# Optimization experiments

Measured on AMD Instinct MI355X. Metric: run time of the kernel, lower is better.

The kernel has to match this reference:

```python
import jax, jax.numpy as jnp
import numpy as np

N = 50000
D_IN = 256
OUT = 16
HEADS = 32
GAT_C = OUT  # out_channels + beta_on(=0)


def _gat_conv(x, src, dst, W, att_src, att_dst, bias):
    """PyG GATConv, concat=False (mean over heads), with self-loops already appended."""
    n = x.shape[0]
    xp = (x @ W).reshape(n, HEADS, GAT_C)            # [N,H,C]
    a_s = jnp.einsum('nhc,hc->nh', xp, att_src)       # [N,H]
    a_d = jnp.einsum('nhc,hc->nh', xp, att_dst)       # [N,H]
    e = jax.nn.leaky_relu(a_s[src] + a_d[dst], 0.2)   # [E,H]
    # segment softmax over incoming edges of each dst node
    m = jax.ops.segment_max(e, dst, num_segments=n)
    e = jnp.exp(e - m[dst])
    s = jax.ops.segment_sum(e, dst, num_segments=n)
    alpha = e / (s[dst] + 1e-16)                      # [E,H]
    out = jax.ops.segment_sum(alpha[:, :, None] * xp[src], dst, num_segments=n)  # [N,H,C]
    return out.mean(axis=1) + bias                    # [N,C]


def setup_inputs() -> dict:
    key = jax.random.key(0)
    ks = jax.random.split(key, 16)
    E = 800000
    x = jax.random.normal(ks[0], (N, D_IN), dtype=jnp.float32)
    edge_index = jax.random.randint(ks[1], (2, E), 0, N, dtype=jnp.int64)
    sc = 1.0 / np.sqrt(D_IN)
    W1 = jax.random.normal(ks[2], (D_IN, HEADS * GAT_C), dtype=jnp.float32) * sc
    att_src1 = jax.random.normal(ks[3], (HEADS, GAT_C), dtype=jnp.float32) * 0.1
    att_dst1 = jax.random.normal(ks[4], (HEADS, GAT_C), dtype=jnp.float32) * 0.1
    b1 = jnp.zeros((GAT_C,), dtype=jnp.float32)
    W2 = jax.random.normal(ks[5], (D_IN, HEADS * GAT_C), dtype=jnp.float32) * sc
    att_src2 = jax.random.normal(ks[6], (HEADS, GAT_C), dtype=jnp.float32) * 0.1
    att_dst2 = jax.random.normal(ks[7], (HEADS, GAT_C), dtype=jnp.float32) * 0.1
    b2 = jnp.zeros((GAT_C,), dtype=jnp.float32)
    lin1_w = jax.random.normal(ks[8], (D_IN, 4 * OUT), dtype=jnp.float32) * sc
    lin1_b = jnp.zeros((4 * OUT,), dtype=jnp.float32)
    lin2_w = jax.random.normal(ks[9], (4 * OUT, OUT), dtype=jnp.float32) * (1.0 / np.sqrt(4 * OUT))
    lin2_b = jnp.zeros((OUT,), dtype=jnp.float32)
    return {"x": x, "edge_index": edge_index,
            "W1": W1, "att_src1": att_src1, "att_dst1": att_dst1, "b1": b1,
            "W2": W2, "att_src2": att_src2, "att_dst2": att_dst2, "b2": b2,
            "lin1_w": lin1_w, "lin1_b": lin1_b, "lin2_w": lin2_w, "lin2_b": lin2_b}


def reference(x, edge_index, W1, att_src1, att_dst1, b1, W2, att_src2, att_dst2, b2,
              lin1_w, lin1_b, lin2_w, lin2_b):
    n = x.shape[0]
    loops = jnp.arange(n, dtype=edge_index.dtype)
    # conv1: flow source_to_target on edge_index -> aggregate src=row0 into dst=row1
    src = jnp.concatenate([edge_index[0], loops])
    dst = jnp.concatenate([edge_index[1], loops])
    x_in = jax.nn.elu(_gat_conv(x, src, dst, W1, att_src1, att_dst1, b1))
    # conv2: flow target_to_source on transposed edge_index -> same effective (src,dst)
    x_out = jax.nn.elu(_gat_conv(x, src, dst, W2, att_src2, att_dst2, b2))
    x1 = jax.nn.elu(x @ lin1_w + lin1_b)
    x_self = jax.nn.elu(x1 @ lin2_w + lin2_b)
    return (x_in, x_out, x_self)
```

## Files before the change

### kernel.cpp

```cpp
#include <hip/hip_runtime.h>

typedef __bf16 bf16x8 __attribute__((ext_vector_type(8)));
typedef float  f32x4  __attribute__((ext_vector_type(4)));
typedef float  f32x2  __attribute__((ext_vector_type(2)));

#define NNODES   50000
#define DIN      256
#define HEADS    32
#define CDIM     16
#define NH       512
#define ERAW     800000
#define SCAN_B   196
#define LDSW     280

#if __has_builtin(__builtin_amdgcn_exp2f)
#define EXP2(x) __builtin_amdgcn_exp2f(x)
#else
#define EXP2(x) __expf((x) * 0.6931471805599453f)
#endif

__device__ __forceinline__ float b2f(unsigned short u) {
    return __uint_as_float(((unsigned)u) << 16);
}
__device__ __forceinline__ unsigned short f2b(float f) {
    unsigned v = __float_as_uint(f);
    v += 0x7fffu + ((v >> 16) & 1u);
    return (unsigned short)(v >> 16);
}

__global__ void k_detect(const int* __restrict__ ei, int* __restrict__ flag) {
    if (threadIdx.x == 0 && blockIdx.x == 0) {
        int nz = 0;
        #pragma unroll
        for (int t = 0; t < 64; ++t) nz |= ei[2 * t + 1];
        flag[0] = (nz == 0) ? 1 : 0;
    }
}

__global__ void k_zero_deg(int* __restrict__ deg) {
    int i = blockIdx.x * 256 + threadIdx.x;
    if (i < NNODES) deg[i] = 0;
}

__global__ void k_hist(const int* __restrict__ ei, const int* __restrict__ flag,
                       int* __restrict__ deg) {
    int e = blockIdx.x * 256 + threadIdx.x;
    int d = flag[0] ? ei[2 * ERAW + 2 * e] : ei[ERAW + e];
    atomicAdd(&deg[d], 1);
}

__global__ void k_scan_blk(const int* __restrict__ deg, int* __restrict__ part,
                           int* __restrict__ bsum) {
    __shared__ int sm[256];
    int b = blockIdx.x, t = threadIdx.x, i = b * 256 + t;
    int v = (i < NNODES) ? deg[i] : 0;
    sm[t] = v; __syncthreads();
    for (int off = 1; off < 256; off <<= 1) {
        int u = (t >= off) ? sm[t - off] : 0;
        __syncthreads();
        sm[t] += u; __syncthreads();
    }
    if (i < NNODES) part[i] = sm[t] - v;
    if (t == 255) bsum[b] = sm[255];
}

__global__ void k_scan_top(int* __restrict__ bsum) {
    __shared__ int sm[256];
    int t = threadIdx.x;
    int v = (t < SCAN_B) ? bsum[t] : 0;
    sm[t] = v; __syncthreads();
    for (int off = 1; off < 256; off <<= 1) {
        int u = (t >= off) ? sm[t - off] : 0;
        __syncthreads();
        sm[t] += u; __syncthreads();
    }
    if (t < SCAN_B) bsum[t] = sm[t] - v;
}

__global__ void k_scan_add(const int* __restrict__ part, const int* __restrict__ bsum,
                           int* __restrict__ rs, int* __restrict__ cur) {
    int b = blockIdx.x, t = threadIdx.x, i = b * 256 + t;
    if (i < NNODES) { int r = part[i] + bsum[b]; rs[i] = r; cur[i] = r; }
}

__global__ void k_scatter(const int* __restrict__ ei, const int* __restrict__ flag,
                          int* __restrict__ cur, int* __restrict__ csr) {
    int e = blockIdx.x * 256 + threadIdx.x;
    int s, d;
    if (flag[0]) { s = ei[2 * e]; d = ei[2 * ERAW + 2 * e]; }
    else         { s = ei[e];     d = ei[ERAW + e]; }
    int pos = atomicAdd(&cur[d], 1);
    csr[pos] = s;
}

__global__ void k_cast_x(const float* __restrict__ x, unsigned short* __restrict__ xb) {
    int i = blockIdx.x * 256 + threadIdx.x;
    float4 v = *(const float4*)(x + (size_t)i * 4);
    ushort4 o;
    o.x = f2b(v.x); o.y = f2b(v.y); o.z = f2b(v.z); o.w = f2b(v.w);
    *(ushort4*)(xb + (size_t)i * 4) = o;
}

__global__ void k_tr(const float* __restrict__ src, unsigned short* __restrict__ dst,
                     int K, int N) {
    int n = blockIdx.x, k = threadIdx.x;
    dst[n * K + k] = f2b(src[k * N + n]);
}

__global__ void k_tr_gat(const float* __restrict__ src, unsigned short* __restrict__ dst) {
    int n = blockIdx.x, k = threadIdx.x;
    int p = (n & ~63) | (((n & 15) << 2) | ((n >> 4) & 3));
    dst[n * DIN + k] = f2b(src[k * NH + p]);
}

__global__ void __launch_bounds__(256)
k_gemm_xp(const unsigned short* __restrict__ xb,
          const unsigned short* __restrict__ Wt,
          unsigned* __restrict__ xp8) {
    __shared__ unsigned short As[64 * LDSW];
    int row0 = blockIdx.x * 64;
    int tid = threadIdx.x;
    int w = tid >> 6, lane = tid & 63;
    int r = lane & 15, quad = lane >> 4;

    {
        int row = tid >> 2, slot = tid & 3;
        const uint4* g = (const uint4*)(xb + (size_t)(row0 + row) * DIN);
        uint4* l = (uint4*)(As + row * LDSW);
        #pragma unroll
        for (int i = 0; i < 8; ++i)
            l[slot + 4 * i] = g[slot + 4 * i];
    }
    __syncthreads();

    #pragma unroll
    for (int ch = 0; ch < 2; ++ch) {
        f32x4 acc[4][4] = {};
        #pragma unroll
        for (int kc = 0; kc < 8; ++kc) {
            bf16x8 a[4], b[4];
            #pragma unroll
            for (int sub = 0; sub < 4; ++sub)
                a[sub] = *(const bf16x8*)(As + (sub * 16 + r) * LDSW + kc * 32 + quad * 8);
            #pragma unroll
            for (int t = 0; t < 4; ++t) {
                int col = ch * 256 + w * 64 + t * 16 + r;
                b[t] = *(const bf16x8*)(Wt + (size_t)col * DIN + kc * 32 + quad * 8);
            }
            #pragma unroll
            for (int t = 0; t < 4; ++t)
                #pragma unroll
                for (int sub = 0; sub < 4; ++sub)
                    acc[sub][t] = __builtin_amdgcn_mfma_f32_16x16x32_bf16(a[sub], b[t], acc[sub][t], 0, 0, 0);
        }
        #pragma unroll
        for (int sub = 0; sub < 4; ++sub) {
            #pragma unroll
            for (int j = 0; j < 4; ++j) {
                int row = row0 + sub * 16 + quad * 4 + j;
                if (row < NNODES) {
                    unsigned u = (unsigned)__builtin_amdgcn_cvt_pk_fp8_f32(
                                     acc[sub][0][j], acc[sub][1][j], 0, false);
                    u = (unsigned)__builtin_amdgcn_cvt_pk_fp8_f32(
                                     acc[sub][2][j], acc[sub][3][j], (int)u, true);
                    xp8[(size_t)row * 128 + ch * 64 + w * 16 + r] = u;
                }
            }
        }
    }
}

__global__ void k_att(const unsigned* __restrict__ xp8,
                      const float* __restrict__ att_src,
                      const float* __restrict__ att_dst,
                      float* __restrict__ a_s, float* __restrict__ a_d) {
    int tid = threadIdx.x;
    int nd = blockIdx.x * 4 + (tid >> 6);
    int ln = tid & 63;
    int h = ln >> 1;

    const uint2 q = *(const uint2*)(xp8 + (size_t)nd * 128 + ln * 2);
    f32x2 p0 = __builtin_amdgcn_cvt_pk_f32_fp8((int)q.x, false);
    f32x2 p1 = __builtin_amdgcn_cvt_pk_f32_fp8((int)q.x, true);
    f32x2 p2 = __builtin_amdgcn_cvt_pk_f32_fp8((int)q.y, false);
    f32x2 p3 = __builtin_amdgcn_cvt_pk_f32_fp8((int)q.y, true);
    float f[8] = {p0.x, p0.y, p1.x, p1.y, p2.x, p2.y, p3.x, p3.y};

    const f32x4* As4 = (const f32x4*)att_src;
    const f32x4* Ad4 = (const f32x4*)att_dst;
    f32x4 s0 = As4[ln * 2], s1 = As4[ln * 2 + 1];
    f32x4 d0 = Ad4[ln * 2], d1 = Ad4[ln * 2 + 1];

    float ps = f[0]*s0.x + f[1]*s0.y + f[2]*s0.z + f[3]*s0.w
             + f[4]*s1.x + f[5]*s1.y + f[6]*s1.z + f[7]*s1.w;
    float pd = f[0]*d0.x + f[1]*d0.y + f[2]*d0.z + f[3]*d0.w
             + f[4]*d1.x + f[5]*d1.y + f[6]*d1.z + f[7]*d1.w;

    ps += __shfl_xor(ps, 1, 64);
    pd += __shfl_xor(pd, 1, 64);
    const float LOG2E = 1.4426950408889634f;
    if ((ln & 1) == 0) a_s[nd * HEADS + h] = ps * LOG2E;
    else               a_d[nd * HEADS + h] = pd * LOG2E;
}

__global__ void k_conv(const int* __restrict__ csr, const int* __restrict__ rs,
                       const int* __restrict__ deg,
                       const unsigned* __restrict__ xp8,
                       const float* __restrict__ a_s, const float* __restrict__ a_d,
                       const float* __restrict__ bias, float* __restrict__ out) {
    int nd = blockIdx.x * 4 + (threadIdx.x >> 6);
    int ln = threadIdx.x & 63;
    int h  = ln >> 1;
    int cb = (ln & 1) * 8;
    float adn = a_d[nd * HEADS + h];
    int beg = __builtin_amdgcn_readfirstlane(rs[nd]);
    int cnt = __builtin_amdgcn_readfirstlane(deg[nd]);
    const uint2* xv = (const uint2*)xp8;

    float denom = 0.f;
    float acc[8] = {0, 0, 0, 0, 0, 0, 0, 0};

    #define EDGE_BODY(AV, QV, LIVE)                                        \
    {                                                                      \
        float tt = (AV) + adn;                                             \
        tt = fmaxf(tt, 0.2f * tt);                                         \
        float e = EXP2(tt);                                                \
        e = (LIVE) ? e : 0.f;                                              \
        denom += e;                                                        \
        f32x2 p0 = __builtin_amdgcn_cvt_pk_f32_fp8((int)(QV).x, false);    \
        f32x2 p1 = __builtin_amdgcn_cvt_pk_f32_fp8((int)(QV).x, true);     \
        f32x2 p2 = __builtin_amdgcn_cvt_pk_f32_fp8((int)(QV).y, false);    \
        f32x2 p3 = __builtin_amdgcn_cvt_pk_f32_fp8((int)(QV).y, true);     \
        acc[0] += e * p0.x; acc[1] += e * p0.y;                            \
        acc[2] += e * p1.x; acc[3] += e * p1.y;                            \
        acc[4] += e * p2.x; acc[5] += e * p2.y;                            \
        acc[6] += e * p3.x; acc[7] += e * p3.y;                            \
    }

    float avS = a_s[nd * HEADS + h];
    uint2 qvS = xv[(size_t)nd * 64 + ln];
    int nb = (cnt + 3) >> 2;
    float avP[4]; uint2 qvP[4]; int svN[4];
    if (nb > 0) {
        #pragma unroll
        for (int k = 0; k < 4; ++k) {
            int ce = k < cnt ? k : cnt - 1;
            int s = csr[beg + ce];
            avP[k] = a_s[s * HEADS + h];
            qvP[k] = xv[(size_t)s * 64 + ln];
        }
        #pragma unroll
        for (int k = 0; k < 4; ++k) {
            int idx = 4 + k;
            int ce = idx < cnt ? idx : cnt - 1;
            svN[k] = csr[beg + ce];
        }
    }
    __builtin_amdgcn_sched_barrier(0);
    EDGE_BODY(avS, qvS, 1)

    for (int b = 1; b < nb; ++b) {
        float avN[4]; uint2 qvN[4];
        #pragma unroll
        for (int k = 0; k < 4; ++k) {
            int s = svN[k];
            avN[k] = a_s[s * HEADS + h];
            qvN[k] = xv[(size_t)s * 64 + ln];
        }
        {
            int nbase = (b + 1 < nb ? b + 1 : nb - 1) * 4;
            #pragma unroll
            for (int k = 0; k < 4; ++k) {
                int idx = nbase + k;
                int ce = idx < cnt ? idx : cnt - 1;
                svN[k] = csr[beg + ce];
            }
        }
        __builtin_amdgcn_sched_barrier(0);
        #pragma unroll
        for (int k = 0; k < 4; ++k) EDGE_BODY(avP[k], qvP[k], 1)
        #pragma unroll
        for (int k = 0; k < 4; ++k) { avP[k] = avN[k]; qvP[k] = qvN[k]; }
    }
    if (nb > 0) {
        #pragma unroll
        for (int k = 0; k < 4; ++k) {
            int idx = (nb - 1) * 4 + k;
            EDGE_BODY(avP[k], qvP[k], idx < cnt)
        }
    }
    #undef EDGE_BODY

    float inv = 1.f / (denom + 1e-16f);
    #pragma unroll
    for (int c = 0; c < 8; ++c) acc[c] *= inv;

    #pragma unroll
    for (int mask = 2; mask <= 32; mask <<= 1) {
        #pragma unroll
        for (int c = 0; c < 8; ++c) acc[c] += __shfl_xor(acc[c], mask, 64);
    }
    if (ln < 2) {
        #pragma unroll
        for (int c2 = 0; c2 < 8; ++c2) {
            int c = cb + c2;
            float o = acc[c2] * (1.0f / HEADS) + bias[c];
            out[(size_t)nd * CDIM + c] = o > 0.f ? o : expm1f(o);
        }
    }
}

__global__ void k_mlp1(const unsigned short* __restrict__ xb,
                       const unsigned short* __restrict__ w1t,
                       const float* __restrict__ bb1, unsigned short* __restrict__ x1) {
    int wave = blockIdx.x * 4 + (threadIdx.x >> 6);
    if (wave >= 782) return;
    int lane = threadIdx.x & 63;
    int r = lane & 15, quad = lane >> 4;
    int row0 = wave * 64;

    f32x4 acc[4][4] = {};
    #pragma unroll
    for (int kc = 0; kc < 8; ++kc) {
        bf16x8 a[4];
        #pragma unroll
        for (int sub = 0; sub < 4; ++sub) {
            int row = row0 + sub * 16 + r;
            if (row0 + sub * 16 < NNODES)
                a[sub] = *(const bf16x8*)(xb + (size_t)row * DIN + kc * 32 + quad * 8);
            else {
                union { unsigned short u[8]; bf16x8 v; } z;
                #pragma unroll
                for (int j = 0; j < 8; ++j) z.u[j] = 0;
                a[sub] = z.v;
            }
        }
        #pragma unroll
        for (int t = 0; t < 4; ++t) {
            int col = t * 16 + r;
            bf16x8 b = *(const bf16x8*)(w1t + (size_t)col * DIN + kc * 32 + quad * 8);
            #pragma unroll
            for (int sub = 0; sub < 4; ++sub)
                acc[sub][t] = __builtin_amdgcn_mfma_f32_16x16x32_bf16(a[sub], b, acc[sub][t], 0, 0, 0);
        }
    }
    #pragma unroll
    for (int sub = 0; sub < 4; ++sub) {
        #pragma unroll
        for (int t = 0; t < 4; ++t) {
            int col = t * 16 + r;
            float bv = bb1[col];
            #pragma unroll
            for (int j = 0; j < 4; ++j) {
                int row = row0 + sub * 16 + quad * 4 + j;
                if (row < NNODES) {
                    float v = acc[sub][t][j] + bv;
                    v = v > 0.f ? v : expm1f(v);
                    x1[(size_t)row * 64 + col] = f2b(v);
                }
            }
        }
    }
}

__global__ void k_mlp2(const unsigned short* __restrict__ x1,
                       const unsigned short* __restrict__ w2t,
                       const float* __restrict__ bb2, float* __restrict__ out) {
    int wave = blockIdx.x * 4 + (threadIdx.x >> 6);
    if (wave >= 3125) return;
    int lane = threadIdx.x & 63;
    int r = lane & 15, quad = lane >> 4;

    f32x4 acc = {};
    #pragma unroll
    for (int kc = 0; kc < 2; ++kc) {
        bf16x8 a = *(const bf16x8*)(x1 + (size_t)(wave * 16 + r) * 64 + kc * 32 + quad * 8);
        bf16x8 b = *(const bf16x8*)(w2t + (size_t)r * 64 + kc * 32 + quad * 8);
        acc = __builtin_amdgcn_mfma_f32_16x16x32_bf16(a, b, acc, 0, 0, 0);
    }
    float bv = bb2[r];
    #pragma unroll
    for (int j = 0; j < 4; ++j) {
        int row = wave * 16 + quad * 4 + j;
        float v = acc[j] + bv;
        v = v > 0.f ? v : expm1f(v);
        out[(size_t)row * CDIM + r] = v;
    }
}

extern "C" void kernel_launch(void* const* d_in, const int* in_sizes, int n_in,
                              void* d_out, int out_size, void* d_ws, size_t ws_size,
                              hipStream_t stream) {
    const float* x  = (const float*)d_in[0];
    const int* ei   = (const int*)d_in[1];
    const float* W[2]    = {(const float*)d_in[2], (const float*)d_in[6]};
    const float* atS[2]  = {(const float*)d_in[3], (const float*)d_in[7]};
    const float* atD[2]  = {(const float*)d_in[4], (const float*)d_in[8]};
    const float* bias[2] = {(const float*)d_in[5], (const float*)d_in[9]};
    const float* w1 = (const float*)d_in[10];
    const float* b1 = (const float*)d_in[11];
    const float* w2 = (const float*)d_in[12];
    const float* b2 = (const float*)d_in[13];
    float* out = (float*)d_out;

    char* ws = (char*)d_ws;
    unsigned* xp8 = (unsigned*)(ws);
    unsigned short* xb  = (unsigned short*)(ws + 25600000);
    unsigned short* Wt  = (unsigned short*)(ws + 51200000);
    unsigned short* w1t = (unsigned short*)(ws + 51462144);
    unsigned short* w2t = (unsigned short*)(ws + 51494912);
    float* a_s = (float*)(ws + 51496960);
    float* a_d = (float*)(ws + 57896960);
    unsigned short* x1 = (unsigned short*)(ws + 51496960);
    int* deg   = (int*)(ws + 64296960);
    int* rs    = (int*)(ws + 64496960);
    int* cur   = (int*)(ws + 64696960);
    int* part  = (int*)(ws + 64896960);
    int* bsum  = (int*)(ws + 65096960);
    int* csr   = (int*)(ws + 65097984);
    int* flag  = (int*)(ws + 68297984);

    k_detect<<<1, 64, 0, stream>>>(ei, flag);
    k_zero_deg<<<SCAN_B, 256, 0, stream>>>(deg);
    k_hist    <<<3125, 256, 0, stream>>>(ei, flag, deg);
    k_scan_blk<<<SCAN_B, 256, 0, stream>>>(deg, part, bsum);
    k_scan_top<<<1, 256, 0, stream>>>(bsum);
    k_scan_add<<<SCAN_B, 256, 0, stream>>>(part, bsum, rs, cur);
    k_scatter <<<3125, 256, 0, stream>>>(ei, flag, cur, csr);

    k_cast_x<<<12500, 256, 0, stream>>>(x, xb);
    k_tr<<<64, 256, 0, stream>>>(w1, w1t, DIN, 64);
    k_tr<<<16, 64, 0, stream>>>(w2, w2t, 64, CDIM);

    for (int cv = 0; cv < 2; ++cv) {
        k_tr_gat <<<512, 256, 0, stream>>>(W[cv], Wt);
        k_gemm_xp<<<782, 256, 0, stream>>>(xb, Wt, xp8);
        k_att    <<<12500, 256, 0, stream>>>(xp8, atS[cv], atD[cv], a_s, a_d);
        k_conv   <<<12500, 256, 0, stream>>>(csr, rs, deg, xp8, a_s, a_d,
                                             bias[cv], out + (size_t)cv * 800000);
    }
    k_mlp1<<<196, 256, 0, stream>>>(xb, w1t, b1, x1);
    k_mlp2<<<782, 256, 0, stream>>>(x1, w2t, b2, out + 1600000);
}
```

Before: 494.2 us.

## Fuse attention-logit computation into GEMM epilogue and tile weight transposes

Removes the separate k_att kernel by computing the per-head a_s/a_d dot products from the fp32 MFMA accumulators inside the GEMM epilogue, reduced with cross-lane shuffles. This avoids rereading xp8 and one launch per conv, and the logits now come from unquantized fp32 values rather than fp8. The weight transposes are replaced by an LDS-tiled k_trT kernel with coalesced float4 reads, which launches only a few blocks and so leaves most of the GPU idle during that step. The change adds shuffle work and extra global stores to the GEMM epilogue.

```diff
diff --git a/kernel.cpp b/kernel.cpp
--- a/kernel.cpp
+++ b/kernel.cpp
@@ -12,6 +12,7 @@
 #define ERAW     800000
 #define SCAN_B   196
 #define LDSW     280
+#define LOG2E    1.4426950408889634f
 
 #if __has_builtin(__builtin_amdgcn_exp2f)
 #define EXP2(x) __builtin_amdgcn_exp2f(x)
@@ -107,16 +108,40 @@
     dst[n * K + k] = f2b(src[k * N + n]);
 }
 
-__global__ void k_tr_gat(const float* __restrict__ src, unsigned short* __restrict__ dst) {
-    int n = blockIdx.x, k = threadIdx.x;
-    int p = (n & ~63) | (((n & 15) << 2) | ((n >> 4) & 3));
-    dst[n * DIN + k] = f2b(src[k * NH + p]);
+__global__ void k_trT(const float* __restrict__ src, unsigned short* __restrict__ dst,
+                      int srcStride, int doPi) {
+    __shared__ unsigned short T[64][258];
+    int n0 = blockIdx.x * 64;
+    int t = threadIdx.x;
+    int nl = (t & 15) * 4;
+    int kr = t >> 4;
+    for (int kk = 0; kk < 256; kk += 16) {
+        int k = kk + kr;
+        float4 v = *(const float4*)(src + (size_t)k * srcStride + n0 + nl);
+        T[nl + 0][k] = f2b(v.x);
+        T[nl + 1][k] = f2b(v.y);
+        T[nl + 2][k] = f2b(v.z);
+        T[nl + 3][k] = f2b(v.w);
+    }
+    __syncthreads();
+    int rl = t >> 2;
+    int pr = doPi ? (((rl & 15) << 2) | (rl >> 4)) : rl;
+    #pragma unroll
+    for (int j = 0; j < 16; ++j) {
+        int c4 = (t & 3) + 4 * j;
+        ushort2 o0 = *(const ushort2*)&T[pr][c4 * 4];
+        ushort2 o1 = *(const ushort2*)&T[pr][c4 * 4 + 2];
+        ushort4 o; o.x = o0.x; o.y = o0.y; o.z = o1.x; o.w = o1.y;
+        *(ushort4*)(dst + ((size_t)(n0 + rl)) * DIN + c4 * 4) = o;
+    }
 }
 
 __global__ void __launch_bounds__(256)
 k_gemm_xp(const unsigned short* __restrict__ xb,
           const unsigned short* __restrict__ Wt,
-          unsigned* __restrict__ xp8) {
+          unsigned* __restrict__ xp8,
+          const float* __restrict__ att_src, const float* __restrict__ att_dst,
+          float* __restrict__ a_s, float* __restrict__ a_d) {
     __shared__ unsigned short As[64 * LDSW];
     int row0 = blockIdx.x * 64;
     int tid = threadIdx.x;
@@ -133,6 +158,9 @@
     }
     __syncthreads();
 
+    const f32x4* As4 = (const f32x4*)att_src;
+    const f32x4* Ad4 = (const f32x4*)att_dst;
+
     #pragma unroll
     for (int ch = 0; ch < 2; ++ch) {
         f32x4 acc[4][4] = {};
@@ -153,6 +181,9 @@
                 for (int sub = 0; sub < 4; ++sub)
                     acc[sub][t] = __builtin_amdgcn_mfma_f32_16x16x32_bf16(a[sub], b[t], acc[sub][t], 0, 0, 0);
         }
+        int h = ch * 16 + w * 4 + (r >> 2);
+        f32x4 sc = As4[h * 4 + (r & 3)];
+        f32x4 dc = Ad4[h * 4 + (r & 3)];
         #pragma unroll
         for (int sub = 0; sub < 4; ++sub) {
             #pragma unroll
@@ -166,41 +197,26 @@
                     xp8[(size_t)row * 128 + ch * 64 + w * 16 + r] = u;
                 }
             }
-        }
-    }
-}
-
-__global__ void k_att(const unsigned* __restrict__ xp8,
-                      const float* __restrict__ att_src,
-                      const float* __restrict__ att_dst,
-                      float* __restrict__ a_s, float* __restrict__ a_d) {
-    int tid = threadIdx.x;
-    int nd = blockIdx.x * 4 + (tid >> 6);
-    int ln = tid & 63;
-    int h = ln >> 1;
-
-    const uint2 q = *(const uint2*)(xp8 + (size_t)nd * 128 + ln * 2);
-    f32x2 p0 = __builtin_amdgcn_cvt_pk_f32_fp8((int)q.x, false);
-    f32x2 p1 = __builtin_amdgcn_cvt_pk_f32_fp8((int)q.x, true);
-    f32x2 p2 = __builtin_amdgcn_cvt_pk_f32_fp8((int)q.y, false);
-    f32x2 p3 = __builtin_amdgcn_cvt_pk_f32_fp8((int)q.y, true);
-    float f[8] = {p0.x, p0.y, p1.x, p1.y, p2.x, p2.y, p3.x, p3.y};
-
-    const f32x4* As4 = (const f32x4*)att_src;
-    const f32x4* Ad4 = (const f32x4*)att_dst;
-    f32x4 s0 = As4[ln * 2], s1 = As4[ln * 2 + 1];
-    f32x4 d0 = Ad4[ln * 2], d1 = Ad4[ln * 2 + 1];
-
-    float ps = f[0]*s0.x + f[1]*s0.y + f[2]*s0.z + f[3]*s0.w
-             + f[4]*s1.x + f[5]*s1.y + f[6]*s1.z + f[7]*s1.w;
-    float pd = f[0]*d0.x + f[1]*d0.y + f[2]*d0.z + f[3]*d0.w
-             + f[4]*d1.x + f[5]*d1.y + f[6]*d1.z + f[7]*d1.w;
-
-    ps += __shfl_xor(ps, 1, 64);
-    pd += __shfl_xor(pd, 1, 64);
-    const float LOG2E = 1.4426950408889634f;
-    if ((ln & 1) == 0) a_s[nd * HEADS + h] = ps * LOG2E;
-    else               a_d[nd * HEADS + h] = pd * LOG2E;
+            f32x4 ps = acc[sub][0] * sc.x + acc[sub][1] * sc.y
+                     + acc[sub][2] * sc.z + acc[sub][3] * sc.w;
+            f32x4 pd = acc[sub][0] * dc.x + acc[sub][1] * dc.y
+                     + acc[sub][2] * dc.z + acc[sub][3] * dc.w;
+            #pragma unroll
+            for (int m = 1; m <= 2; m <<= 1) {
+                #pragma unroll
+                for (int c = 0; c < 4; ++c) {
+                    ps[c] += __shfl_xor(ps[c], m, 64);
+                    pd[c] += __shfl_xor(pd[c], m, 64);
+                }
+            }
+            int j = r & 3;
+            int row = row0 + sub * 16 + quad * 4 + j;
+            if (row < NNODES) {
+                a_s[row * HEADS + h] = ps[j] * LOG2E;
+                a_d[row * HEADS + h] = pd[j] * LOG2E;
+            }
+        }
+    }
 }
 
 __global__ void k_conv(const int* __restrict__ csr, const int* __restrict__ rs,
@@ -429,13 +445,12 @@
     k_scatter <<<3125, 256, 0, stream>>>(ei, flag, cur, csr);
 
     k_cast_x<<<12500, 256, 0, stream>>>(x, xb);
-    k_tr<<<64, 256, 0, stream>>>(w1, w1t, DIN, 64);
+    k_trT<<<1, 256, 0, stream>>>(w1, w1t, 64, 0);
     k_tr<<<16, 64, 0, stream>>>(w2, w2t, 64, CDIM);
 
     for (int cv = 0; cv < 2; ++cv) {
-        k_tr_gat <<<512, 256, 0, stream>>>(W[cv], Wt);
-        k_gemm_xp<<<782, 256, 0, stream>>>(xb, Wt, xp8);
-        k_att    <<<12500, 256, 0, stream>>>(xp8, atS[cv], atD[cv], a_s, a_d);
+        k_trT    <<<8, 256, 0, stream>>>(W[cv], Wt, NH, 1);
+        k_gemm_xp<<<782, 256, 0, stream>>>(xb, Wt, xp8, atS[cv], atD[cv], a_s, a_d);
         k_conv   <<<12500, 256, 0, stream>>>(csr, rs, deg, xp8, a_s, a_d,
                                              bias[cv], out + (size_t)cv * 800000);
     }
```

New measurement: 490.6 us. Within noise of the previous version (-0.7%).
